# Performance work log

Hardware: AMD Instinct MI355X
Metric: run time of the kernel (lower is better)

Reference implementation:

```python
import jax, jax.numpy as jnp
import numpy as np

# Production-scale dims (see shape_source)
B, N_C, N_T = 2, 4096, 1024
D_X, D_S = 64, 3
K = 32                 # SGNP default k=32
RECALL = 0.95          # approx_min_k recall_target as in approx_knn
SX = SS = ST = 1.0     # scale_x_sim / scale_s_sim / scale_t_sim


def setup_inputs() -> dict:
    key = jax.random.key(0)
    ks = jax.random.split(key, 6)
    return {
        "x_ctx": jax.random.normal(ks[0], (B, N_C, D_X), jnp.float32),
        "s_ctx": jax.random.normal(ks[1], (B, N_C, D_S), jnp.float32),
        "t_ctx": jax.random.uniform(ks[2], (B, N_C, 1), dtype=jnp.float32),
        "mask_ctx": jnp.ones((B, N_C), dtype=bool),
        "x_test": jax.random.normal(ks[3], (B, N_T, D_X), jnp.float32),
        "s_test": jax.random.normal(ks[4], (B, N_T, D_S), jnp.float32),
        "t_test": jax.random.uniform(ks[5], (B, N_T, 1), dtype=jnp.float32),
    }


def _sq_cdist(q, r):
    # squared euclidean distance, [B,Nq,d] x [B,Nr,d] -> [B,Nq,Nr]
    qn = jnp.sum(q * q, axis=-1)
    rn = jnp.sum(r * r, axis=-1)
    return qn[:, :, None] + rn[:, None, :] - 2.0 * jnp.einsum("bqd,brd->bqr", q, r)


def _knn(qx, qs, qt, rx, rs, rt, mask):
    """Vectorized approx_knn: multi-modal distances, causal mask, top-k, gather."""
    inf = jnp.inf
    m = mask[:, None, :]                       # [B,1,Nr] -> masked refs get inf (as _safe_mask)
    d_x = jnp.where(m, _sq_cdist(qx, rx), inf)  # [B,Nq,Nr]
    d_s = jnp.where(m, _sq_cdist(qs, rs), inf)
    d_t = rt[:, None, :, 0] - qt[:, :, None, 0]  # signed time diff (r - q)
    d_t = jnp.where(m, d_t, inf)
    d_t = jnp.where(d_t <= 0, d_t, inf)          # causal_t mask
    d_sq = (SX * d_x) ** 2 + (SS * d_s) ** 2 + (ST * d_t) ** 2
    _, idx = jax.lax.approx_min_k(jax.lax.stop_gradient(d_sq), K, recall_target=RECALL)
    g = lambda d: jnp.take_along_axis(d, idx, axis=-1)  # [B,Nq,K]
    return idx, g(d_x), g(d_s), g(d_t)


def reference(x_ctx, s_ctx, t_ctx, mask_ctx, x_test, s_test, t_test):
    # ctx->ctx and test->ctx kNN (build_graph)
    idx_cc, dx_cc, ds_cc, dt_cc = _knn(x_ctx, s_ctx, t_ctx, x_ctx, s_ctx, t_ctx, mask_ctx)
    idx_ct, dx_ct, ds_ct, dt_ct = _knn(x_test, s_test, t_test, x_ctx, s_ctx, t_ctx, mask_ctx)

    # batch offsets into the flat node array [B*N_C ctx nodes, then B*N_T test nodes]
    off = jnp.arange(B) * N_C
    senders_cc = idx_cc.reshape(-1) + jnp.repeat(off, N_C * K)
    senders_ct = idx_ct.reshape(-1) + jnp.repeat(off, N_T * K)
    senders = jnp.concatenate([senders_cc, senders_ct])
    receivers = jnp.repeat(jnp.arange(B * (N_C + N_T)), K)

    cat = lambda a, b: jnp.concatenate([a.reshape(-1), b.reshape(-1)])
    d_x = cat(dx_cc, dx_ct)   # [B*(N_C+N_T)*K]
    d_s = cat(ds_cc, ds_ct)
    d_t = cat(dt_cc, dt_ct)
    edge_mask = jnp.isfinite(d_x) & jnp.isfinite(d_s) & jnp.isfinite(d_t)
    return senders, receivers, d_x, d_s, d_t, edge_mask
```

## Files before the change

kernel.cpp:

```cpp
#include <hip/hip_runtime.h>

namespace {
constexpr int kB  = 2;
constexpr int kNC = 4096;
constexpr int kNT = 1024;
constexpr int kDX = 64;
constexpr int kK  = 32;
constexpr int kNQ = kB * (kNC + kNT);
constexpr int kQPB2 = kNC + kNT;
constexpr long long kE = (long long)kNQ * kK;
constexpr int QPW  = 4;
constexpr int WAVES = 4;
constexpr int QPB  = WAVES * QPW;
constexpr int TILE = 64;
constexpr int HALF = 2048;
constexpr int NGRP = kNQ / QPB;
constexpr int GPB  = NGRP / kB;
constexpr float kBigFinite = 1e30f;
constexpr size_t kOffRn    = 0;
constexpr size_t kOffPermR = 32768;
constexpr size_t kOffPrefR = 65536;
constexpr size_t kOffCntR  = 67840;
constexpr size_t kOffPrefQ = 69888;
constexpr size_t kOffCntQ  = 72192;
constexpr size_t kOffQperm = 74240;
constexpr size_t kOffKeys  = 115200;
constexpr size_t kOffXp    = 5358080;
constexpr size_t kOffMs    = 13746688;
constexpr size_t kOffMr    = 13877760;
constexpr size_t kWsNeed   = kOffMr + (size_t)kB * kNC * 8;
}

__device__ __forceinline__ int tbucket(float t) {
    int b = (int)(t * 256.0f);
    return b < 0 ? 0 : (b > 255 ? 255 : b);
}

__device__ __forceinline__ void resolve_q(int gid,
    const float* x_ctx, const float* s_ctx, const float* t_ctx,
    const float* x_test, const float* s_test, const float* t_test,
    int& b, const float*& qx, const float*& qs, const float*& qt)
{
    if (gid < kB * kNC) {
        b  = gid >> 12;
        qx = x_ctx + (size_t)gid * kDX;
        qs = s_ctx + (size_t)gid * 3;
        qt = t_ctx + gid;
    } else {
        const int g2 = gid - kB * kNC;
        b  = g2 >> 10;
        qx = x_test + (size_t)g2 * kDX;
        qs = s_test + (size_t)g2 * 3;
        qt = t_test + g2;
    }
}

__device__ __forceinline__ void insert_half(unsigned long long& listKey,
    unsigned long long keyQ, int lane, int base)
{
    const unsigned long long thr = __shfl(listKey, base + 31, 64);
    unsigned long long hb = __ballot(keyQ < thr);
    while (hb) {
        const int srcl = __ffsll((unsigned long long)hb) - 1;
        hb &= hb - 1;
        const unsigned long long K = __shfl(keyQ, srcl, 64);
        const unsigned long long lt = __ballot(listKey < K);
        const unsigned int half = base ? (unsigned int)(lt >> 32)
                                       : (unsigned int)lt;
        const int pos = __popc(half) + base;
        if (pos < base + 32) {
            const unsigned long long up = __shfl_up(listKey, 1, 64);
            if (lane >= base && lane < base + 32) {
                if (lane > pos)       listKey = up;
                else if (lane == pos) listKey = K;
            }
        }
    }
}

__global__ __launch_bounds__(256)
void prep_rn(const float* __restrict__ x, float* __restrict__ rn_ws)
{
    const int r = blockIdx.x * 256 + threadIdx.x;
    const float4* xr = (const float4*)(x + (size_t)r * kDX);
    float rn = 0.f;
    #pragma unroll
    for (int j = 0; j < 16; ++j) {
        const float4 rv = xr[j];
        rn = fmaf(rv.x, rv.x, rn); rn = fmaf(rv.y, rv.y, rn);
        rn = fmaf(rv.z, rv.z, rn); rn = fmaf(rv.w, rv.w, rn);
    }
    rn_ws[r] = rn;
}

__global__ __launch_bounds__(256)
void prep_zero(int* __restrict__ cntR, int* __restrict__ cntQ)
{
    const int i = blockIdx.x * 256 + threadIdx.x;
    if (i < 512) cntR[i] = 0;
    else         cntQ[i - 512] = 0;
}

__global__ __launch_bounds__(256)
void prep_hist(const float* __restrict__ t_ctx, const float* __restrict__ t_test,
               int* __restrict__ cntR, int* __restrict__ cntQ)
{
    const int i = blockIdx.x * 256 + threadIdx.x;
    if (i < 8192) {
        const int b = i >> 12;
        atomicAdd(&cntR[b * 256 + tbucket(t_ctx[i])], 1);
    } else {
        const int gid = i - 8192;
        const int b = (gid < kB * kNC) ? (gid >> 12) : ((gid - kB * kNC) >> 10);
        const float qt = (gid < kB * kNC) ? t_ctx[gid] : t_test[gid - kB * kNC];
        atomicAdd(&cntQ[b * 256 + tbucket(qt)], 1);
    }
}

__global__ __launch_bounds__(256)
void prep_prefix(int* __restrict__ cntR, int* __restrict__ cntQ,
                 int* __restrict__ prefR, int* __restrict__ prefQ)
{
    __shared__ int sh[256];
    const int blk = blockIdx.x;
    int* cnt  = (blk < 2) ? (cntR  + blk * 256) : (cntQ  + (blk - 2) * 256);
    int* pref = (blk < 2) ? (prefR + blk * 257) : (prefQ + (blk - 2) * 257);
    const int tid = threadIdx.x;
    sh[tid] = cnt[tid];
    __syncthreads();
    if (tid == 0) {
        int acc = 0;
        for (int i = 0; i < 256; ++i) { const int v = sh[i]; sh[i] = acc; acc += v; }
        pref[256] = acc;
    }
    __syncthreads();
    pref[tid] = sh[tid];
    cnt[tid]  = sh[tid];
}

__global__ __launch_bounds__(256)
void prep_scatter(const float* __restrict__ t_ctx, const float* __restrict__ t_test,
                  int* __restrict__ cntR, int* __restrict__ cntQ,
                  int* __restrict__ permR, int* __restrict__ qperm)
{
    const int i = blockIdx.x * 256 + threadIdx.x;
    if (i < 8192) {
        const int b = i >> 12, rl = i & (kNC - 1);
        const int pos = atomicAdd(&cntR[b * 256 + tbucket(t_ctx[i])], 1);
        permR[b * kNC + pos] = rl;
    } else {
        const int gid = i - 8192;
        const int b = (gid < kB * kNC) ? (gid >> 12) : ((gid - kB * kNC) >> 10);
        const float qt = (gid < kB * kNC) ? t_ctx[gid] : t_test[gid - kB * kNC];
        const int pos = atomicAdd(&cntQ[b * 256 + tbucket(qt)], 1);
        qperm[b * kQPB2 + pos] = gid;
    }
}

__global__ __launch_bounds__(256)
void prep_permute(const float* __restrict__ x_ctx, const float* __restrict__ s_ctx,
                  const float* __restrict__ t_ctx, const unsigned char* __restrict__ mask_ctx,
                  const float* __restrict__ rn_ws, const int* __restrict__ permR,
                  float4* __restrict__ xp4, float4* __restrict__ msrt,
                  int2* __restrict__ mrn)
{
    const int n   = blockIdx.x * 256 + threadIdx.x;
    const int b   = n >> 16;
    const int rem = n & 65535;
    const int pos = rem >> 4, col = rem & 15;
    const int o   = permR[b * kNC + pos];
    xp4[n] = ((const float4*)x_ctx)[(size_t)b * kNC * 16 + (size_t)o * 16 + col];
    if (col == 0) {
        const float* rs = s_ctx + ((size_t)b * kNC + o) * 3;
        const float rtv = t_ctx[b * kNC + o];
        msrt[b * kNC + pos] = make_float4(rs[0], rs[1], rs[2], rtv);
        const bool m = (mask_ctx[b * kNC + o] != 0);
        const float rn = rn_ws[b * kNC + o];
        mrn[b * kNC + pos] = make_int2(
            m ? __float_as_int(rn) : __float_as_int(__builtin_inff()), o);
    }
}

__global__ __launch_bounds__(256, 4)
void knn_v8_part(const float* __restrict__ x_ctx, const float* __restrict__ s_ctx,
                 const float* __restrict__ t_ctx,
                 const float* __restrict__ x_test, const float* __restrict__ s_test,
                 const float* __restrict__ t_test,
                 const float4* __restrict__ xp4g, const float4* __restrict__ msrtg,
                 const int2* __restrict__ mrng,
                 const int* __restrict__ prefR, const int* __restrict__ qperm,
                 unsigned long long* __restrict__ keys)
{
    __shared__ float4 xt[2][TILE * 16];
    __shared__ int wred[WAVES];

    const int tid  = threadIdx.x;
    const int lane = tid & 63;
    const int w    = __builtin_amdgcn_readfirstlane(tid >> 6);
    const int blk  = blockIdx.x;
    const int gidx = (NGRP - 1) - (blk >> 1);
    const int h    = blk & 1;
    const int b    = (gidx >= GPB) ? 1 : 0;
    const int gg   = gidx - b * GPB;

    const int* qpm = qperm + b * kQPB2 + gg * QPB;
    int gid_q[QPW];
    #pragma unroll
    for (int q = 0; q < QPW; ++q) gid_q[q] = qpm[w * QPW + q];

    const float4* xp4  = xp4g  + (size_t)b * kNC * 16;
    const float4* msrt = msrtg + (size_t)b * kNC;
    const int2*   mrn  = mrng  + (size_t)b * kNC;
    const int*    pf   = prefR + b * 257;

    const float* qxp[QPW];
    float qs0[QPW], qs1[QPW], qs2[QPW], qsn[QPW], qtv[QPW], qn[QPW];
    #pragma unroll
    for (int q = 0; q < QPW; ++q) {
        int bb; const float *qx, *qs, *qt;
        resolve_q(gid_q[q], x_ctx, s_ctx, t_ctx, x_test, s_test, t_test,
                  bb, qx, qs, qt);
        qxp[q] = qx;
        qs0[q] = qs[0]; qs1[q] = qs[1]; qs2[q] = qs[2]; qtv[q] = qt[0];
        qsn[q] = qs0[q]*qs0[q] + qs1[q]*qs1[q] + qs2[q]*qs2[q];
        const float ql = qx[lane];
        float s = ql * ql;
        #pragma unroll
        for (int off = 32; off > 0; off >>= 1) s += __shfl_xor(s, off, 64);
        qn[q] = s;
    }

    int vmax = 0;
    #pragma unroll
    for (int q = 0; q < QPW; ++q) {
        const int qb = tbucket(qtv[q]);
        int bound = pf[qb + 1];
        if (pf[qb] < kK) bound = kNC;
        vmax = bound > vmax ? bound : vmax;
    }
    if (lane == 0) wred[w] = vmax;
    __syncthreads();
    int bmax = wred[0];
    #pragma unroll
    for (int i = 1; i < WAVES; ++i) bmax = wred[i] > bmax ? wred[i] : bmax;

    const int lo = h * HALF;
    const int hi = bmax < lo + HALF ? bmax : lo + HALF;
    const int ntile = (hi > lo) ? ((hi - lo + TILE - 1) >> 6) : 0;
    const size_t hbase = (size_t)lo * 16;

    int sg[4], ss[4];
    #pragma unroll
    for (int i = 0; i < 4; ++i) {
        const int n = tid + 256 * i;
        const int r = n >> 4, j = n & 15;
        sg[i] = n;
        ss[i] = (r << 4) | (j ^ (r & 7));
    }
    if (ntile > 0) {
        #pragma unroll
        for (int i = 0; i < 4; ++i) xt[0][ss[i]] = xp4[hbase + sg[i]];
    }
    __syncthreads();

    const int lbase = lane << 4, lsw = lane & 7;
    const float INF = __builtin_inff();
    unsigned long long lst01 = ~0ull, lst23 = ~0ull;

    for (int t = 0; t < ntile; ++t) {
        float4 p0, p1, p2, p3;
        const bool pre = (t + 1 < ntile);
        if (pre) {
            const size_t nb = hbase + (size_t)(t + 1) * 1024;
            p0 = xp4[nb + sg[0]]; p1 = xp4[nb + sg[1]];
            p2 = xp4[nb + sg[2]]; p3 = xp4[nb + sg[3]];
        }
        const float4* buf = xt[t & 1];

        float dot[QPW] = {0.f, 0.f, 0.f, 0.f};
        #pragma unroll
        for (int j = 0; j < 16; ++j) {
            const float4 rv = buf[lbase | (j ^ lsw)];
            #pragma unroll
            for (int q = 0; q < QPW; ++q) {
                const float4 qv = ((const float4*)qxp[q])[j];
                dot[q] = fmaf(qv.x, rv.x, dot[q]);
                dot[q] = fmaf(qv.y, rv.y, dot[q]);
                dot[q] = fmaf(qv.z, rv.z, dot[q]);
                dot[q] = fmaf(qv.w, rv.w, dot[q]);
            }
        }

        const int pos = lo + t * TILE + lane;
        const float4 ms = msrt[pos];
        const int2   mr = mrn[pos];
        const float rs0 = ms.x, rs1 = ms.y, rs2 = ms.z, rtv = ms.w;
        const float rn  = __int_as_float(mr.x);
        const int   o   = mr.y;
        const float rsn = rs0*rs0 + rs1*rs1 + rs2*rs2;

        #pragma unroll
        for (int q = 0; q < QPW; ++q) {
            float d_x = qn[q] + rn - 2.0f * dot[q];
            const float sdot = qs0[q]*rs0 + qs1[q]*rs1 + qs2[q]*rs2;
            float d_s = qsn[q] + rsn - 2.0f * sdot;
            float d_t = rtv - qtv[q];
            if (!(d_t <= 0.f)) d_t = INF;
            const float v = d_x*d_x + d_s*d_s + d_t*d_t;
            const unsigned long long key =
                ((unsigned long long)__float_as_uint(v) << 32) | (unsigned)o;
            if (q < 2) insert_half(lst01, key, lane, (q & 1) * 32);
            else       insert_half(lst23, key, lane, (q & 1) * 32);
        }

        if (pre) {
            float4* nbuf = xt[(t + 1) & 1];
            nbuf[ss[0]] = p0; nbuf[ss[1]] = p1;
            nbuf[ss[2]] = p2; nbuf[ss[3]] = p3;
        }
        __syncthreads();
    }

    #pragma unroll
    for (int p = 0; p < 2; ++p) {
        const unsigned long long key = p ? lst23 : lst01;
        const int gsel = (lane < 32) ? gid_q[2*p] : gid_q[2*p+1];
        keys[((size_t)gsel * 2 + h) * 32 + (lane & 31)] = key;
    }
}

__global__ __launch_bounds__(256)
void knn_v5_merge(const float* __restrict__ x_ctx, const float* __restrict__ s_ctx,
                  const float* __restrict__ t_ctx, const unsigned char* __restrict__ mask_ctx,
                  const float* __restrict__ x_test, const float* __restrict__ s_test,
                  const float* __restrict__ t_test,
                  const unsigned long long* __restrict__ keys,
                  float* __restrict__ out)
{
    __shared__ unsigned long long kbuf[WAVES][64];
    __shared__ unsigned long long merged[WAVES][32];

    const int tid  = threadIdx.x;
    const int lane = tid & 63;
    const int w    = tid >> 6;
    const int qid  = blockIdx.x * WAVES + w;

    int b; const float *qx, *qs, *qt;
    resolve_q(qid, x_ctx, s_ctx, t_ctx, x_test, s_test, t_test, b, qx, qs, qt);
    const float qs0_ = qs[0], qs1_ = qs[1], qs2_ = qs[2], qtv_ = qt[0];
    const float qsn_ = qs0_*qs0_ + qs1_*qs1_ + qs2_*qs2_;
    const float ql = qx[lane];
    float qn_ = ql * ql;
    #pragma unroll
    for (int off = 32; off > 0; off >>= 1) qn_ += __shfl_xor(qn_, off, 64);

    const unsigned long long mykey = keys[(size_t)qid * 64 + lane];
    kbuf[w][lane] = mykey;
    __syncthreads();

    int cnt = 0;
    const int ob = (lane < 32) ? 32 : 0;
    #pragma unroll
    for (int j = 0; j < 32; ++j) cnt += (kbuf[w][ob + j] < mykey) ? 1 : 0;
    const int pos = (lane & 31) + cnt;
    if (pos < 32) merged[w][pos] = mykey;
    __syncthreads();

    if (lane < kK) {
        const unsigned long long key = merged[w][lane];
        const int rsel = (int)(key & 0xFFFFFFFFull);

        const float*  rsp = s_ctx + (size_t)b * kNC * 3;
        const float*  rtp = t_ctx + (size_t)b * kNC;
        const unsigned char* mp = mask_ctx + (size_t)b * kNC;

        const float4* xr = (const float4*)(x_ctx + ((size_t)b * kNC + rsel) * kDX);
        const float4* qr = (const float4*)qx;
        float dot = 0.f, rn2 = 0.f;
        #pragma unroll
        for (int j = 0; j < 16; ++j) {
            const float4 rv = xr[j];
            const float4 qv = qr[j];
            rn2 = fmaf(rv.x, rv.x, rn2); rn2 = fmaf(rv.y, rv.y, rn2);
            rn2 = fmaf(rv.z, rv.z, rn2); rn2 = fmaf(rv.w, rv.w, rn2);
            dot = fmaf(qv.x, rv.x, dot); dot = fmaf(qv.y, rv.y, dot);
            dot = fmaf(qv.z, rv.z, dot); dot = fmaf(qv.w, rv.w, dot);
        }
        float d_x = qn_ + rn2 - 2.0f * dot;
        const float rs0 = rsp[rsel*3+0], rs1 = rsp[rsel*3+1], rs2 = rsp[rsel*3+2];
        const float rsn = rs0*rs0 + rs1*rs1 + rs2*rs2;
        const float sdot = qs0_*rs0 + qs1_*rs1 + qs2_*rs2;
        float d_s = qsn_ + rsn - 2.0f * sdot;
        const float dt_raw = rtp[rsel] - qtv_;
        const bool  m = (mp[rsel] != 0);
        const bool  causal = m && (dt_raw <= 0.f);

        const float em = causal ? 1.0f : 0.0f;
        const float d_x_out = m ? d_x : kBigFinite;
        const float d_s_out = m ? d_s : kBigFinite;
        const float d_t_out = causal ? dt_raw : kBigFinite;

        const size_t e = (size_t)qid * kK + (size_t)lane;
        out[e]                = (float)(rsel + b * kNC);
        out[(size_t)kE   + e] = (float)qid;
        out[(size_t)kE*2 + e] = d_x_out;
        out[(size_t)kE*3 + e] = d_s_out;
        out[(size_t)kE*4 + e] = d_t_out;
        out[(size_t)kE*5 + e] = em;
    }
}

__global__ __launch_bounds__(256, 4)
void knn_v4(const float* __restrict__ x_ctx, const float* __restrict__ s_ctx,
            const float* __restrict__ t_ctx, const unsigned char* __restrict__ mask_ctx,
            const float* __restrict__ x_test, const float* __restrict__ s_test,
            const float* __restrict__ t_test, float* __restrict__ out)
{
    __shared__ float4 xt[2][TILE * 16];
    const int tid  = threadIdx.x;
    const int lane = tid & 63;
    const int w    = __builtin_amdgcn_readfirstlane(tid >> 6);
    const int qbase = blockIdx.x * QPB;
    const int gid0  = qbase + w * QPW;
    int b;
    { int b_; const float *a, *c, *d;
      resolve_q(qbase, x_ctx, s_ctx, t_ctx, x_test, s_test, t_test, b_, a, c, d);
      b = b_; }
    const float4* xb4 = (const float4*)x_ctx + (size_t)b * kNC * (kDX / 4);
    const float*  rsp = s_ctx + (size_t)b * kNC * 3;
    const float*  rtp = t_ctx + (size_t)b * kNC;
    const unsigned char* mp = mask_ctx + (size_t)b * kNC;
    const float* qxp[QPW];
    float qs0[QPW], qs1[QPW], qs2[QPW], qsn[QPW], qtv[QPW], qn[QPW];
    #pragma unroll
    for (int q = 0; q < QPW; ++q) {
        int bb; const float *qx, *qs, *qt;
        resolve_q(gid0 + q, x_ctx, s_ctx, t_ctx, x_test, s_test, t_test, bb, qx, qs, qt);
        qxp[q] = qx;
        qs0[q] = qs[0]; qs1[q] = qs[1]; qs2[q] = qs[2]; qtv[q] = qt[0];
        qsn[q] = qs0[q]*qs0[q] + qs1[q]*qs1[q] + qs2[q]*qs2[q];
        const float ql = qx[lane];
        float s = ql * ql;
        #pragma unroll
        for (int off = 32; off > 0; off >>= 1) s += __shfl_xor(s, off, 64);
        qn[q] = s;
    }
    int sg[4], ss[4];
    #pragma unroll
    for (int i = 0; i < 4; ++i) {
        const int n = tid + 256 * i;
        const int r = n >> 4, j = n & 15;
        sg[i] = n; ss[i] = (r << 4) | (j ^ (r & 7));
    }
    #pragma unroll
    for (int i = 0; i < 4; ++i) xt[0][ss[i]] = xb4[sg[i]];
    __syncthreads();
    const int lbase = lane << 4, lsw = lane & 7;
    const float INF = __builtin_inff();
    unsigned long long lst01 = ~0ull, lst23 = ~0ull;
    for (int t = 0; t < kNC / TILE; ++t) {
        float4 p0, p1, p2, p3;
        const bool pre = (t + 1 < kNC / TILE);
        if (pre) {
            const size_t nb = (size_t)(t + 1) * 1024;
            p0 = xb4[nb + sg[0]]; p1 = xb4[nb + sg[1]];
            p2 = xb4[nb + sg[2]]; p3 = xb4[nb + sg[3]];
        }
        const float4* buf = xt[t & 1];
        float dot[QPW] = {0.f, 0.f, 0.f, 0.f};
        float rn = 0.f;
        #pragma unroll
        for (int j = 0; j < 16; ++j) {
            const float4 rv = buf[lbase | (j ^ lsw)];
            rn = fmaf(rv.x, rv.x, rn); rn = fmaf(rv.y, rv.y, rn);
            rn = fmaf(rv.z, rv.z, rn); rn = fmaf(rv.w, rv.w, rn);
            #pragma unroll
            for (int q = 0; q < QPW; ++q) {
                const float4 qv = ((const float4*)qxp[q])[j];
                dot[q] = fmaf(qv.x, rv.x, dot[q]);
                dot[q] = fmaf(qv.y, rv.y, dot[q]);
                dot[q] = fmaf(qv.z, rv.z, dot[q]);
                dot[q] = fmaf(qv.w, rv.w, dot[q]);
            }
        }
        const int r = t * TILE + lane;
        const float rs0 = rsp[r*3+0], rs1 = rsp[r*3+1], rs2 = rsp[r*3+2];
        const float rtv = rtp[r];
        const bool  m   = (mp[r] != 0);
        const float rsn = rs0*rs0 + rs1*rs1 + rs2*rs2;
        #pragma unroll
        for (int q = 0; q < QPW; ++q) {
            float d_x = qn[q] + rn - 2.0f * dot[q];
            const float sdot = qs0[q]*rs0 + qs1[q]*rs1 + qs2[q]*rs2;
            float d_s = qsn[q] + rsn - 2.0f * sdot;
            float d_t = rtv - qtv[q];
            if (!m) { d_x = INF; d_s = INF; d_t = INF; }
            if (!(d_t <= 0.f)) d_t = INF;
            const float v = d_x*d_x + d_s*d_s + d_t*d_t;
            const unsigned long long key =
                ((unsigned long long)__float_as_uint(v) << 32) | (unsigned)r;
            if (q < 2) insert_half(lst01, key, lane, (q & 1) * 32);
            else       insert_half(lst23, key, lane, (q & 1) * 32);
        }
        if (pre) {
            float4* nbuf = xt[(t + 1) & 1];
            nbuf[ss[0]] = p0; nbuf[ss[1]] = p1;
            nbuf[ss[2]] = p2; nbuf[ss[3]] = p3;
        }
        __syncthreads();
    }
    #pragma unroll
    for (int p = 0; p < 2; ++p) {
        const unsigned long long myl = p ? lst23 : lst01;
        const int qidx = 2 * p + (lane >> 5);
        const int rsel = (int)(myl & 0xFFFFFFFFull);
        const int gid  = gid0 + qidx;
        const float* qx  = (lane < 32) ? qxp[2*p] : qxp[2*p+1];
        const float qn_  = (lane < 32) ? qn [2*p] : qn [2*p+1];
        const float qs0_ = (lane < 32) ? qs0[2*p] : qs0[2*p+1];
        const float qs1_ = (lane < 32) ? qs1[2*p] : qs1[2*p+1];
        const float qs2_ = (lane < 32) ? qs2[2*p] : qs2[2*p+1];
        const float qsn_ = (lane < 32) ? qsn[2*p] : qsn[2*p+1];
        const float qtv_ = (lane < 32) ? qtv[2*p] : qtv[2*p+1];
        const float4* xr = (const float4*)(x_ctx + ((size_t)b * kNC + rsel) * kDX);
        const float4* qr = (const float4*)qx;
        float dot = 0.f, rn2 = 0.f;
        #pragma unroll
        for (int j = 0; j < 16; ++j) {
            const float4 rv = xr[j];
            const float4 qv = qr[j];
            rn2 = fmaf(rv.x, rv.x, rn2); rn2 = fmaf(rv.y, rv.y, rn2);
            rn2 = fmaf(rv.z, rv.z, rn2); rn2 = fmaf(rv.w, rv.w, rn2);
            dot = fmaf(qv.x, rv.x, dot); dot = fmaf(qv.y, rv.y, dot);
            dot = fmaf(qv.z, rv.z, dot); dot = fmaf(qv.w, rv.w, dot);
        }
        float d_x = qn_ + rn2 - 2.0f * dot;
        const float rs0 = rsp[rsel*3+0], rs1 = rsp[rsel*3+1], rs2 = rsp[rsel*3+2];
        const float rsn = rs0*rs0 + rs1*rs1 + rs2*rs2;
        const float sdot = qs0_*rs0 + qs1_*rs1 + qs2_*rs2;
        float d_s = qsn_ + rsn - 2.0f * sdot;
        const float dt_raw = rtp[rsel] - qtv_;
        const bool  m = (mp[rsel] != 0);
        const bool  causal = m && (dt_raw <= 0.f);
        const float em = causal ? 1.0f : 0.0f;
        const size_t e = (size_t)gid * kK + (size_t)(lane & 31);
        out[e]                = (float)(rsel + b * kNC);
        out[(size_t)kE   + e] = (float)gid;
        out[(size_t)kE*2 + e] = m ? d_x : kBigFinite;
        out[(size_t)kE*3 + e] = m ? d_s : kBigFinite;
        out[(size_t)kE*4 + e] = causal ? dt_raw : kBigFinite;
        out[(size_t)kE*5 + e] = em;
    }
}

extern "C" void kernel_launch(void* const* d_in, const int* in_sizes, int n_in,
                              void* d_out, int out_size, void* d_ws, size_t ws_size,
                              hipStream_t stream) {
    (void)in_sizes; (void)n_in; (void)out_size;
    const float* x_ctx = (const float*)d_in[0];
    const float* s_ctx = (const float*)d_in[1];
    const float* t_ctx = (const float*)d_in[2];
    const unsigned char* mask_ctx = (const unsigned char*)d_in[3];
    const float* x_test = (const float*)d_in[4];
    const float* s_test = (const float*)d_in[5];
    const float* t_test = (const float*)d_in[6];

    if (ws_size >= kWsNeed) {
        char* ws = (char*)d_ws;
        float* rn_ws = (float*)(ws + kOffRn);
        int*   permR = (int*)(ws + kOffPermR);
        int*   prefR = (int*)(ws + kOffPrefR);
        int*   cntR  = (int*)(ws + kOffCntR);
        int*   prefQ = (int*)(ws + kOffPrefQ);
        int*   cntQ  = (int*)(ws + kOffCntQ);
        int*   qperm = (int*)(ws + kOffQperm);
        unsigned long long* keys = (unsigned long long*)(ws + kOffKeys);
        float4* xp4  = (float4*)(ws + kOffXp);
        float4* msrt = (float4*)(ws + kOffMs);
        int2*   mrn  = (int2*)(ws + kOffMr);

        prep_zero   <<<dim3(4),   dim3(256), 0, stream>>>(cntR, cntQ);
        prep_rn     <<<dim3(32),  dim3(256), 0, stream>>>(x_ctx, rn_ws);
        prep_hist   <<<dim3(72),  dim3(256), 0, stream>>>(t_ctx, t_test, cntR, cntQ);
        prep_prefix <<<dim3(4),   dim3(256), 0, stream>>>(cntR, cntQ, prefR, prefQ);
        prep_scatter<<<dim3(72),  dim3(256), 0, stream>>>(t_ctx, t_test, cntR, cntQ,
                                                          permR, qperm);
        prep_permute<<<dim3(512), dim3(256), 0, stream>>>(x_ctx, s_ctx, t_ctx,
                                                          mask_ctx, rn_ws, permR,
                                                          xp4, msrt, mrn);
        knn_v8_part <<<dim3(2 * NGRP), dim3(256), 0, stream>>>(
            x_ctx, s_ctx, t_ctx, x_test, s_test, t_test,
            xp4, msrt, mrn, prefR, qperm, keys);
        knn_v5_merge<<<dim3(kNQ / WAVES), dim3(256), 0, stream>>>(
            x_ctx, s_ctx, t_ctx, mask_ctx, x_test, s_test, t_test, keys,
            (float*)d_out);
    } else {
        knn_v4<<<dim3(kNQ / QPB), dim3(256), 0, stream>>>(
            x_ctx, s_ctx, t_ctx, mask_ctx, x_test, s_test, t_test, (float*)d_out);
    }
}
```

Measured before the change: 425.8 us.

## Fuse split kNN partial and merge kernels into single full-range kernel

Drops the two-halves split of the reference range along with the separate merge kernel. Each block now scans the whole causally bounded range for its queries and writes the final edges directly. A masked-valid histogram prefix (prefV) is added so the early-cutoff test counts only valid references, and blocks interleave the two batches. This removes the 64-bit key round-trip through memory and one launch, but leaves half as many blocks, each doing longer serial work, which reduces parallelism.

```diff
diff --git a/kernel.cpp b/kernel.cpp
--- a/kernel.cpp
+++ b/kernel.cpp
@@ -13,7 +13,6 @@
 constexpr int WAVES = 4;
 constexpr int QPB  = WAVES * QPW;
 constexpr int TILE = 64;
-constexpr int HALF = 2048;
 constexpr int NGRP = kNQ / QPB;
 constexpr int GPB  = NGRP / kB;
 constexpr float kBigFinite = 1e30f;
@@ -21,14 +20,15 @@
 constexpr size_t kOffPermR = 32768;
 constexpr size_t kOffPrefR = 65536;
 constexpr size_t kOffCntR  = 67840;
-constexpr size_t kOffPrefQ = 69888;
-constexpr size_t kOffCntQ  = 72192;
-constexpr size_t kOffQperm = 74240;
-constexpr size_t kOffKeys  = 115200;
-constexpr size_t kOffXp    = 5358080;
-constexpr size_t kOffMs    = 13746688;
-constexpr size_t kOffMr    = 13877760;
-constexpr size_t kWsNeed   = kOffMr + (size_t)kB * kNC * 8;
+constexpr size_t kOffPrefV = 69888;
+constexpr size_t kOffCntV  = 72192;
+constexpr size_t kOffPrefQ = 74240;
+constexpr size_t kOffCntQ  = 76544;
+constexpr size_t kOffQperm = 78592;
+constexpr size_t kOffXp    = 119552;
+constexpr size_t kOffMs    = 8508160;
+constexpr size_t kOffMr    = 8639232;
+constexpr size_t kWsNeed   = 8704768;
 }
 
 __device__ __forceinline__ int tbucket(float t) {
@@ -94,21 +94,27 @@
 }
 
 __global__ __launch_bounds__(256)
-void prep_zero(int* __restrict__ cntR, int* __restrict__ cntQ)
+void prep_zero(int* __restrict__ cntR, int* __restrict__ cntV,
+               int* __restrict__ cntQ)
 {
     const int i = blockIdx.x * 256 + threadIdx.x;
-    if (i < 512) cntR[i] = 0;
-    else         cntQ[i - 512] = 0;
+    if (i < 512)       cntR[i] = 0;
+    else if (i < 1024) cntV[i - 512] = 0;
+    else               cntQ[i - 1024] = 0;
 }
 
 __global__ __launch_bounds__(256)
 void prep_hist(const float* __restrict__ t_ctx, const float* __restrict__ t_test,
-               int* __restrict__ cntR, int* __restrict__ cntQ)
+               const unsigned char* __restrict__ mask_ctx,
+               int* __restrict__ cntR, int* __restrict__ cntV,
+               int* __restrict__ cntQ)
 {
     const int i = blockIdx.x * 256 + threadIdx.x;
     if (i < 8192) {
         const int b = i >> 12;
-        atomicAdd(&cntR[b * 256 + tbucket(t_ctx[i])], 1);
+        const int bkt = tbucket(t_ctx[i]);
+        atomicAdd(&cntR[b * 256 + bkt], 1);
+        if (mask_ctx[i] != 0) atomicAdd(&cntV[b * 256 + bkt], 1);
     } else {
         const int gid = i - 8192;
         const int b = (gid < kB * kNC) ? (gid >> 12) : ((gid - kB * kNC) >> 10);
@@ -118,13 +124,19 @@
 }
 
 __global__ __launch_bounds__(256)
-void prep_prefix(int* __restrict__ cntR, int* __restrict__ cntQ,
-                 int* __restrict__ prefR, int* __restrict__ prefQ)
+void prep_prefix(int* __restrict__ cntR, int* __restrict__ cntV,
+                 int* __restrict__ cntQ,
+                 int* __restrict__ prefR, int* __restrict__ prefV,
+                 int* __restrict__ prefQ)
 {
     __shared__ int sh[256];
     const int blk = blockIdx.x;
-    int* cnt  = (blk < 2) ? (cntR  + blk * 256) : (cntQ  + (blk - 2) * 256);
-    int* pref = (blk < 2) ? (prefR + blk * 257) : (prefQ + (blk - 2) * 257);
+    int* cnt  = (blk < 2) ? (cntR  + blk * 256)
+              : (blk < 4) ? (cntV  + (blk - 2) * 256)
+                          : (cntQ  + (blk - 4) * 256);
+    int* pref = (blk < 2) ? (prefR + blk * 257)
+              : (blk < 4) ? (prefV + (blk - 2) * 257)
+                          : (prefQ + (blk - 4) * 257);
     const int tid = threadIdx.x;
     sh[tid] = cnt[tid];
     __syncthreads();
@@ -182,26 +194,23 @@
 }
 
 __global__ __launch_bounds__(256, 4)
-void knn_v8_part(const float* __restrict__ x_ctx, const float* __restrict__ s_ctx,
-                 const float* __restrict__ t_ctx,
-                 const float* __restrict__ x_test, const float* __restrict__ s_test,
-                 const float* __restrict__ t_test,
-                 const float4* __restrict__ xp4g, const float4* __restrict__ msrtg,
-                 const int2* __restrict__ mrng,
-                 const int* __restrict__ prefR, const int* __restrict__ qperm,
-                 unsigned long long* __restrict__ keys)
+void knn_v9(const float* __restrict__ x_ctx, const float* __restrict__ s_ctx,
+            const float* __restrict__ t_ctx, const unsigned char* __restrict__ mask_ctx,
+            const float* __restrict__ x_test, const float* __restrict__ s_test,
+            const float* __restrict__ t_test,
+            const float4* __restrict__ xp4g, const float4* __restrict__ msrtg,
+            const int2* __restrict__ mrng,
+            const int* __restrict__ prefR, const int* __restrict__ prefV,
+            const int* __restrict__ qperm, float* __restrict__ out)
 {
     __shared__ float4 xt[2][TILE * 16];
-    __shared__ int wred[WAVES];
 
     const int tid  = threadIdx.x;
     const int lane = tid & 63;
     const int w    = __builtin_amdgcn_readfirstlane(tid >> 6);
     const int blk  = blockIdx.x;
-    const int gidx = (NGRP - 1) - (blk >> 1);
-    const int h    = blk & 1;
-    const int b    = (gidx >= GPB) ? 1 : 0;
-    const int gg   = gidx - b * GPB;
+    const int b    = blk & 1;
+    const int gg   = (GPB - 1) - (blk >> 1);
 
     const int* qpm = qperm + b * kQPB2 + gg * QPB;
     int gid_q[QPW];
@@ -212,6 +221,19 @@
     const float4* msrt = msrtg + (size_t)b * kNC;
     const int2*   mrn  = mrng  + (size_t)b * kNC;
     const int*    pf   = prefR + b * 257;
+    const int*    pfv  = prefV + b * 257;
+
+    int bmax = 0;
+    #pragma unroll
+    for (int i = 0; i < QPB; ++i) {
+        const int gq = qpm[i];
+        const float qt = (gq < kB * kNC) ? t_ctx[gq] : t_test[gq - kB * kNC];
+        const int qb = tbucket(qt);
+        int bound = pf[qb + 1];
+        if (pfv[qb] < kK) bound = kNC;
+        bmax = bound > bmax ? bound : bmax;
+    }
+    const int ntile = (bmax + TILE - 1) >> 6;
 
     const float* qxp[QPW];
     float qs0[QPW], qs1[QPW], qs2[QPW], qsn[QPW], qtv[QPW], qn[QPW];
@@ -230,25 +252,6 @@
         qn[q] = s;
     }
 
-    int vmax = 0;
-    #pragma unroll
-    for (int q = 0; q < QPW; ++q) {
-        const int qb = tbucket(qtv[q]);
-        int bound = pf[qb + 1];
-        if (pf[qb] < kK) bound = kNC;
-        vmax = bound > vmax ? bound : vmax;
-    }
-    if (lane == 0) wred[w] = vmax;
-    __syncthreads();
-    int bmax = wred[0];
-    #pragma unroll
-    for (int i = 1; i < WAVES; ++i) bmax = wred[i] > bmax ? wred[i] : bmax;
-
-    const int lo = h * HALF;
-    const int hi = bmax < lo + HALF ? bmax : lo + HALF;
-    const int ntile = (hi > lo) ? ((hi - lo + TILE - 1) >> 6) : 0;
-    const size_t hbase = (size_t)lo * 16;
-
     int sg[4], ss[4];
     #pragma unroll
     for (int i = 0; i < 4; ++i) {
@@ -257,10 +260,8 @@
         sg[i] = n;
         ss[i] = (r << 4) | (j ^ (r & 7));
     }
-    if (ntile > 0) {
-        #pragma unroll
-        for (int i = 0; i < 4; ++i) xt[0][ss[i]] = xp4[hbase + sg[i]];
-    }
+    #pragma unroll
+    for (int i = 0; i < 4; ++i) xt[0][ss[i]] = xp4[sg[i]];
     __syncthreads();
 
     const int lbase = lane << 4, lsw = lane & 7;
@@ -271,7 +272,7 @@
         float4 p0, p1, p2, p3;
         const bool pre = (t + 1 < ntile);
         if (pre) {
-            const size_t nb = hbase + (size_t)(t + 1) * 1024;
+            const size_t nb = (size_t)(t + 1) * 1024;
             p0 = xp4[nb + sg[0]]; p1 = xp4[nb + sg[1]];
             p2 = xp4[nb + sg[2]]; p3 = xp4[nb + sg[3]];
         }
@@ -291,7 +292,7 @@
             }
         }
 
-        const int pos = lo + t * TILE + lane;
+        const int pos = t * TILE + lane;
         const float4 ms = msrt[pos];
         const int2   mr = mrn[pos];
         const float rs0 = ms.x, rs1 = ms.y, rs2 = ms.z, rtv = ms.w;
@@ -321,58 +322,22 @@
         __syncthreads();
     }
 
+    const float*  rsp = s_ctx + (size_t)b * kNC * 3;
+    const float*  rtp = t_ctx + (size_t)b * kNC;
+    const unsigned char* mp = mask_ctx + (size_t)b * kNC;
     #pragma unroll
     for (int p = 0; p < 2; ++p) {
-        const unsigned long long key = p ? lst23 : lst01;
-        const int gsel = (lane < 32) ? gid_q[2*p] : gid_q[2*p+1];
-        keys[((size_t)gsel * 2 + h) * 32 + (lane & 31)] = key;
-    }
-}
-
-__global__ __launch_bounds__(256)
-void knn_v5_merge(const float* __restrict__ x_ctx, const float* __restrict__ s_ctx,
-                  const float* __restrict__ t_ctx, const unsigned char* __restrict__ mask_ctx,
-                  const float* __restrict__ x_test, const float* __restrict__ s_test,
-                  const float* __restrict__ t_test,
-                  const unsigned long long* __restrict__ keys,
-                  float* __restrict__ out)
-{
-    __shared__ unsigned long long kbuf[WAVES][64];
-    __shared__ unsigned long long merged[WAVES][32];
-
-    const int tid  = threadIdx.x;
-    const int lane = tid & 63;
-    const int w    = tid >> 6;
-    const int qid  = blockIdx.x * WAVES + w;
-
-    int b; const float *qx, *qs, *qt;
-    resolve_q(qid, x_ctx, s_ctx, t_ctx, x_test, s_test, t_test, b, qx, qs, qt);
-    const float qs0_ = qs[0], qs1_ = qs[1], qs2_ = qs[2], qtv_ = qt[0];
-    const float qsn_ = qs0_*qs0_ + qs1_*qs1_ + qs2_*qs2_;
-    const float ql = qx[lane];
-    float qn_ = ql * ql;
-    #pragma unroll
-    for (int off = 32; off > 0; off >>= 1) qn_ += __shfl_xor(qn_, off, 64);
-
-    const unsigned long long mykey = keys[(size_t)qid * 64 + lane];
-    kbuf[w][lane] = mykey;
-    __syncthreads();
-
-    int cnt = 0;
-    const int ob = (lane < 32) ? 32 : 0;
-    #pragma unroll
-    for (int j = 0; j < 32; ++j) cnt += (kbuf[w][ob + j] < mykey) ? 1 : 0;
-    const int pos = (lane & 31) + cnt;
-    if (pos < 32) merged[w][pos] = mykey;
-    __syncthreads();
-
-    if (lane < kK) {
-        const unsigned long long key = merged[w][lane];
-        const int rsel = (int)(key & 0xFFFFFFFFull);
-
-        const float*  rsp = s_ctx + (size_t)b * kNC * 3;
-        const float*  rtp = t_ctx + (size_t)b * kNC;
-        const unsigned char* mp = mask_ctx + (size_t)b * kNC;
+        const unsigned long long myl = p ? lst23 : lst01;
+        const int qidx = 2 * p + (lane >> 5);
+        const int rsel = (int)(myl & 0xFFFFFFFFull);
+        const int gid  = gid_q[qidx];
+        const float* qx  = (lane < 32) ? qxp[2*p] : qxp[2*p+1];
+        const float qn_  = (lane < 32) ? qn [2*p] : qn [2*p+1];
+        const float qs0_ = (lane < 32) ? qs0[2*p] : qs0[2*p+1];
+        const float qs1_ = (lane < 32) ? qs1[2*p] : qs1[2*p+1];
+        const float qs2_ = (lane < 32) ? qs2[2*p] : qs2[2*p+1];
+        const float qsn_ = (lane < 32) ? qsn[2*p] : qsn[2*p+1];
+        const float qtv_ = (lane < 32) ? qtv[2*p] : qtv[2*p+1];
 
         const float4* xr = (const float4*)(x_ctx + ((size_t)b * kNC + rsel) * kDX);
         const float4* qr = (const float4*)qx;
@@ -400,9 +365,9 @@
         const float d_s_out = m ? d_s : kBigFinite;
         const float d_t_out = causal ? dt_raw : kBigFinite;
 
-        const size_t e = (size_t)qid * kK + (size_t)lane;
+        const size_t e = (size_t)gid * kK + (size_t)(lane & 31);
         out[e]                = (float)(rsel + b * kNC);
-        out[(size_t)kE   + e] = (float)qid;
+        out[(size_t)kE   + e] = (float)gid;
         out[(size_t)kE*2 + e] = d_x_out;
         out[(size_t)kE*3 + e] = d_s_out;
         out[(size_t)kE*4 + e] = d_t_out;
@@ -571,29 +536,29 @@
         int*   permR = (int*)(ws + kOffPermR);
         int*   prefR = (int*)(ws + kOffPrefR);
         int*   cntR  = (int*)(ws + kOffCntR);
+        int*   prefV = (int*)(ws + kOffPrefV);
+        int*   cntV  = (int*)(ws + kOffCntV);
         int*   prefQ = (int*)(ws + kOffPrefQ);
         int*   cntQ  = (int*)(ws + kOffCntQ);
         int*   qperm = (int*)(ws + kOffQperm);
-        unsigned long long* keys = (unsigned long long*)(ws + kOffKeys);
         float4* xp4  = (float4*)(ws + kOffXp);
         float4* msrt = (float4*)(ws + kOffMs);
         int2*   mrn  = (int2*)(ws + kOffMr);
 
-        prep_zero   <<<dim3(4),   dim3(256), 0, stream>>>(cntR, cntQ);
+        prep_zero   <<<dim3(6),   dim3(256), 0, stream>>>(cntR, cntV, cntQ);
         prep_rn     <<<dim3(32),  dim3(256), 0, stream>>>(x_ctx, rn_ws);
-        prep_hist   <<<dim3(72),  dim3(256), 0, stream>>>(t_ctx, t_test, cntR, cntQ);
-        prep_prefix <<<dim3(4),   dim3(256), 0, stream>>>(cntR, cntQ, prefR, prefQ);
+        prep_hist   <<<dim3(72),  dim3(256), 0, stream>>>(t_ctx, t_test, mask_ctx,
+                                                          cntR, cntV, cntQ);
+        prep_prefix <<<dim3(6),   dim3(256), 0, stream>>>(cntR, cntV, cntQ,
+                                                          prefR, prefV, prefQ);
         prep_scatter<<<dim3(72),  dim3(256), 0, stream>>>(t_ctx, t_test, cntR, cntQ,
                                                           permR, qperm);
         prep_permute<<<dim3(512), dim3(256), 0, stream>>>(x_ctx, s_ctx, t_ctx,
                                                           mask_ctx, rn_ws, permR,
                                                           xp4, msrt, mrn);
-        knn_v8_part <<<dim3(2 * NGRP), dim3(256), 0, stream>>>(
-            x_ctx, s_ctx, t_ctx, x_test, s_test, t_test,
-            xp4, msrt, mrn, prefR, qperm, keys);
-        knn_v5_merge<<<dim3(kNQ / WAVES), dim3(256), 0, stream>>>(
-            x_ctx, s_ctx, t_ctx, mask_ctx, x_test, s_test, t_test, keys,
-            (float*)d_out);
+        knn_v9      <<<dim3(NGRP), dim3(256), 0, stream>>>(
+            x_ctx, s_ctx, t_ctx, mask_ctx, x_test, s_test, t_test,
+            xp4, msrt, mrn, prefR, prefV, qperm, (float*)d_out);
     } else {
         knn_v4<<<dim3(kNQ / QPB), dim3(256), 0, stream>>>(
             x_ctx, s_ctx, t_ctx, mask_ctx, x_test, s_test, t_test, (float*)d_out);
```

Result: faster. 359.9 us (-15.5%).
